# Kernel optimization log

Measured on AMD Instinct MI355X. Metric: run time of the kernel, lower is better.

## Reference

```python
import jax, jax.numpy as jnp
import numpy as np

V_K = 1.0
SIGMA = 0.1
EPS = 1e-10


def setup_inputs() -> dict:
    key = jax.random.key(0)
    ks = jax.random.split(key, 5)
    M, L, N, d, H = 2, 6, 512, 2, 64
    data = jax.random.normal(ks[0], (M, L, N, d), dtype=jnp.float32)
    t_snapshots = jnp.arange(L, dtype=jnp.float32) * 0.1
    w1 = jax.random.normal(ks[1], (H,), dtype=jnp.float32) * 0.5
    b1 = jnp.zeros((H,), jnp.float32)
    W2 = jax.random.normal(ks[2], (H, H), dtype=jnp.float32) / np.float32(np.sqrt(H))
    b2 = jnp.zeros((H,), jnp.float32)
    w3 = jax.random.normal(ks[3], (H,), dtype=jnp.float32) / np.float32(np.sqrt(H))
    b3 = jnp.zeros((), jnp.float32)
    return {"data": data, "t_snapshots": t_snapshots, "w1": w1, "b1": b1,
            "W2": W2, "b2": b2, "w3": w3, "b3": b3}


def _phi(r, w1, b1, W2, b2, w3, b3):
    # scalar-to-scalar tanh MLP applied elementwise to r (any shape)
    h1 = jnp.tanh(r[..., None] * w1 + b1)                      # [..., H]
    h2 = jnp.tanh(jnp.einsum('...h,hk->...k', h1, W2) + b2)    # [..., H]
    return jnp.einsum('...k,k->...', h2, w3) + b3              # [...]


def _loss(data, t, params):
    M, L, N, d = data.shape
    diff = data[:, :, :, None, :] - data[:, :, None, :, :]     # [M,L,N,N,d]
    ssq = jnp.sum(diff * diff, axis=-1)                        # [M,L,N,N]
    dist = jnp.where(ssq > 0, jnp.sqrt(jnp.where(ssq > 0, ssq, 1.0)), 0.0)
    off_diag = ~jnp.eye(N, dtype=bool)                         # [N,N]

    f = lambda r: _phi(r, *params)
    # Phi values on all L snapshots (for energy)
    phi = f(dist)                                              # [M,L,N,N]
    # First/second radial derivatives on current snapshots only (ell = 0..L-2)
    r_cur = dist[:, :-1]                                       # [M,L-1,N,N]
    df = lambda r: jax.jvp(f, (r,), (jnp.ones_like(r),))[1]
    dphi = df(r_cur)                                           # Phi'(r)
    d2phi = jax.jvp(df, (r_cur,), (jnp.ones_like(r_cur),))[1]  # Phi''(r)

    dt = t[1:] - t[:-1]                                        # [L-1]

    # --- drift / dissipation ---
    dist_safe = jnp.maximum(r_cur, EPS)
    unit = diff[:, :-1] / dist_safe[..., None]                 # [M,L-1,N,N,d]
    gphi = jnp.where(off_diag[..., None], dphi[..., None] * unit, 0.0)
    grad_Phi_mean = gphi.sum(axis=3) / N                       # [M,L-1,N,d]
    drift = -V_K * data[:, :-1] - grad_Phi_mean
    total_diss = ((drift ** 2).sum(axis=(2, 3)) / N * dt).sum()

    # --- laplacian / diffusion ---
    lap_phi_mean = jnp.where(off_diag, d2phi, 0.0).sum(axis=-1) / N  # [M,L-1,N]
    lap_sum = V_K * d + lap_phi_mean
    total_diff = (SIGMA ** 2 * lap_sum.mean(axis=-1) * dt).sum()

    # --- energy per snapshot ---
    V_mean = 0.5 * V_K * (data ** 2).sum(axis=-1).mean(axis=-1)      # [M,L]
    Phi_mean = jnp.where(off_diag, phi, 0.0).sum(axis=(-1, -2)) / (N * N)
    E = V_mean + Phi_mean                                            # [M,L]
    total_energy_change = (E[:, 1:] - E[:, :-1]).sum()

    n_pairs = M * (L - 1)
    residual = (total_diss + total_diff - 2.0 * total_energy_change) / n_pairs
    return residual ** 2


def reference(data, t_snapshots, w1, b1, W2, b2, w3, b3):
    return _loss(data, t_snapshots, (w1, b1, W2, b2, w3, b3))
```

## Files before the change

kernel.cpp:

```cpp
#include <hip/hip_runtime.h>
#include <hip/hip_bf16.h>

#define MM 2
#define LL 6
#define NN 512
#define HH 64
#define K_TAB 1024
#define RMAX 16.0f
#define H_STEP (RMAX / (float)K_TAB)
#define HINV   ((float)K_TAB / RMAX)


__device__ __forceinline__ float wave_reduce_sum(float v) {
    #pragma unroll
    for (int m = 32; m > 0; m >>= 1) v += __shfl_xor(v, m, 64);
    return v;
}

__global__ __launch_bounds__(256) void build_nodes(
        const float* __restrict__ w1, const float* __restrict__ b1,
        const float* __restrict__ W2, const float* __restrict__ b2,
        const float* __restrict__ w3, const float* __restrict__ b3,
        float2* __restrict__ nodes, float* __restrict__ acc) {
    int gid  = blockIdx.x * blockDim.x + threadIdx.x;
    int wave = gid >> 6;
    int lane = gid & 63;
    if (gid < 64) acc[gid] = 0.0f;
    if (wave > K_TAB) return;

    float r = (float)wave * H_STEP;

    float w1l = w1[lane];
    float u   = fmaf(r, w1l, b1[lane]);
    float t1  = tanhf(u);
    float e1  = 1.0f - t1 * t1;
    float h1  = t1;
    float h1p = e1 * w1l;

    float v = b2[lane], vp = 0.0f;
    #pragma unroll
    for (int h = 0; h < HH; ++h) {
        float a  = __shfl(h1,  h, 64);
        float ap = __shfl(h1p, h, 64);
        float w  = W2[h * HH + lane];
        v  = fmaf(a,  w, v);
        vp = fmaf(ap, w, vp);
    }
    float t2 = tanhf(v);
    float e2 = 1.0f - t2 * t2;
    float w3l = w3[lane];
    float phik = w3l * t2;
    float dpk  = w3l * e2 * vp;

    float sphi = wave_reduce_sum(phik);
    float sdp  = wave_reduce_sum(dpk);
    if (lane == 0)
        nodes[wave] = make_float2(sphi + b3[0], sdp * H_STEP);
}

__global__ __launch_bounds__(256) void pair_kernel(
        const float* __restrict__ data, const float2* __restrict__ nodes,
        float* __restrict__ acc) {
    const int blocks_per_ml = NN / 4;
    int ml = blockIdx.x / blocks_per_ml;
    int i4 = blockIdx.x % blocks_per_ml;

    __shared__ float4 coef[K_TAB];
    __shared__ float2 xs[NN];
    __shared__ float  red[4 * 4];

    #pragma unroll
    for (int e = threadIdx.x, it = 0; it < K_TAB / 256; ++it, e += 256) {
        float2 g0 = nodes[e];
        float2 g1 = nodes[e + 1];
        float  d  = g1.x - g0.x;
        coef[e] = make_float4(g0.x, g0.y,
                              3.0f * d - 2.0f * g0.y - g1.y,
                              g0.y + g1.y - 2.0f * d);
    }
    {
        const float4* src = (const float4*)(data + (size_t)ml * NN * 2);
        ((float4*)xs)[threadIdx.x] = src[threadIdx.x];
    }
    __syncthreads();

    int wv   = threadIdx.x >> 6;
    int lane = threadIdx.x & 63;
    int i    = i4 * 4 + wv;
    float2 xi = xs[i];

    float aphi = 0.0f, ad2 = 0.0f, agx = 0.0f, agy = 0.0f;
    #pragma unroll
    for (int jj = 0; jj < NN / 64; ++jj) {
        int j = jj * 64 + lane;
        float2 xj = xs[j];
        float dx = xi.x - xj.x;
        float dy = xi.y - xj.y;
        float ssq = fmaf(dx, dx, dy * dy);
        float rr  = sqrtf(ssq);
        float f   = rr * HINV;
        int   idx = (int)f;
        idx = idx > (K_TAB - 1) ? (K_TAB - 1) : idx;
        float t = f - (float)idx;
        float4 c = coef[idx];
        float phi  = fmaf(t, fmaf(t, fmaf(t, c.w, c.z), c.y), c.x);
        float dph  = fmaf(t, fmaf(t, 3.0f * c.w, 2.0f * c.z), c.y) * HINV;
        float d2ph = fmaf(t, 6.0f * c.w, 2.0f * c.z) * (HINV * HINV);
        float inv_r = 1.0f / fmaxf(rr, 1e-10f);
        bool off = (j != i);
        aphi += off ? phi  : 0.0f;
        ad2  += off ? d2ph : 0.0f;
        float s = dph * inv_r;
        agx = fmaf(s, dx, agx);
        agy = fmaf(s, dy, agy);
    }

    aphi = wave_reduce_sum(aphi);
    ad2  = wave_reduce_sum(ad2);
    agx  = wave_reduce_sum(agx);
    agy  = wave_reduce_sum(agy);

    if (lane == 0) {
        const float invN = 1.0f / (float)NN;
        float driftx = -xi.x - agx * invN;
        float drifty = -xi.y - agy * invN;
        float dr2 = fmaf(driftx, driftx, drifty * drifty);
        float vsq = fmaf(xi.x, xi.x, xi.y * xi.y);
        red[wv * 4 + 0] = aphi;
        red[wv * 4 + 1] = ad2;
        red[wv * 4 + 2] = dr2;
        red[wv * 4 + 3] = vsq;
    }
    __syncthreads();
    if (threadIdx.x < 4) {
        float s = red[0 * 4 + threadIdx.x] + red[1 * 4 + threadIdx.x]
                + red[2 * 4 + threadIdx.x] + red[3 * 4 + threadIdx.x];
        atomicAdd(&acc[ml * 4 + threadIdx.x], s);
    }
}

__global__ void finalize(const float* __restrict__ acc,
                         const float* __restrict__ t,
                         float* __restrict__ out) {
    if (threadIdx.x != 0 || blockIdx.x != 0) return;
    const double N = (double)NN;
    const double SIG2 = 0.01;
    const double VKD  = 2.0;
    double diss = 0.0, diffu = 0.0, dE = 0.0;
    for (int m = 0; m < MM; ++m) {
        double E0 = 0.0;
        for (int l = 0; l < LL; ++l) {
            int ml = m * LL + l;
            double sphi = (double)acc[ml * 4 + 0];
            double sd2  = (double)acc[ml * 4 + 1];
            double sdr  = (double)acc[ml * 4 + 2];
            double sv   = (double)acc[ml * 4 + 3];
            double E = 0.5 * sv / N + sphi / (N * N);
            if (l == 0) E0 = E;
            if (l == LL - 1) dE += E - E0;
            if (l < LL - 1) {
                double dt = (double)t[l + 1] - (double)t[l];
                diss  += sdr / N * dt;
                diffu += SIG2 * (VKD + sd2 / (N * N)) * dt;
            }
        }
    }
    double res = (diss + diffu - 2.0 * dE) / (double)(MM * (LL - 1));
    out[0] = (float)(res * res);
}

extern "C" void kernel_launch(void* const* d_in, const int* in_sizes, int n_in,
                              void* d_out, int out_size, void* d_ws, size_t ws_size,
                              hipStream_t stream) {
    const float* data = (const float*)d_in[0];
    const float* t    = (const float*)d_in[1];
    const float* w1   = (const float*)d_in[2];
    const float* b1   = (const float*)d_in[3];
    const float* W2   = (const float*)d_in[4];
    const float* b2   = (const float*)d_in[5];
    const float* w3   = (const float*)d_in[6];
    const float* b3   = (const float*)d_in[7];

    float2* nodes = (float2*)d_ws;
    float*  acc   = (float*)((char*)d_ws + 16384);

    build_nodes<<<257, 256, 0, stream>>>(w1, b1, W2, b2, w3, b3, nodes, acc);
    pair_kernel<<<MM * LL * (NN / 4), 256, 0, stream>>>(data, nodes, acc);
    finalize<<<1, 64, 0, stream>>>(acc, t, (float*)d_out);
}
```

Before: 87.38 us.

## Fuse finalize into pair kernel via last-block ticket and halve spline table

Removes the separate finalize launch by having the last pair-kernel block, found through an atomic ticket counter, compute the final scalar. The cubic Hermite table also shrinks from 1024 to 512 nodes, which halves the build_nodes work and the per-block shared-memory coefficient fill. In exchange, each block does one extra atomic and a fence, and the coarser spline lowers interpolation accuracy for phi and its derivatives.

```diff
diff --git a/kernel.cpp b/kernel.cpp
--- a/kernel.cpp
+++ b/kernel.cpp
@@ -5,7 +5,7 @@
 #define LL 6
 #define NN 512
 #define HH 64
-#define K_TAB 1024
+#define K_TAB 512
 #define RMAX 16.0f
 #define H_STEP (RMAX / (float)K_TAB)
 #define HINV   ((float)K_TAB / RMAX)
@@ -21,14 +21,16 @@
         const float* __restrict__ w1, const float* __restrict__ b1,
         const float* __restrict__ W2, const float* __restrict__ b2,
         const float* __restrict__ w3, const float* __restrict__ b3,
-        float2* __restrict__ nodes, float* __restrict__ acc) {
+        float2* __restrict__ nodes, float* __restrict__ acc,
+        int* __restrict__ ticket) {
     int gid  = blockIdx.x * blockDim.x + threadIdx.x;
-    int wave = gid >> 6;
+    int node = gid >> 6;
     int lane = gid & 63;
     if (gid < 64) acc[gid] = 0.0f;
-    if (wave > K_TAB) return;
+    if (gid == 64) *ticket = 0;
+    if (node > K_TAB) return;
 
-    float r = (float)wave * H_STEP;
+    float r = (float)node * H_STEP;
 
     float w1l = w1[lane];
     float u   = fmaf(r, w1l, b1[lane]);
@@ -49,18 +51,16 @@
     float t2 = tanhf(v);
     float e2 = 1.0f - t2 * t2;
     float w3l = w3[lane];
-    float phik = w3l * t2;
-    float dpk  = w3l * e2 * vp;
-
-    float sphi = wave_reduce_sum(phik);
-    float sdp  = wave_reduce_sum(dpk);
+    float sphi = wave_reduce_sum(w3l * t2);
+    float sdp  = wave_reduce_sum(w3l * e2 * vp);
     if (lane == 0)
-        nodes[wave] = make_float2(sphi + b3[0], sdp * H_STEP);
+        nodes[node] = make_float2(sphi + b3[0], sdp * H_STEP);
 }
 
 __global__ __launch_bounds__(256) void pair_kernel(
         const float* __restrict__ data, const float2* __restrict__ nodes,
-        float* __restrict__ acc) {
+        const float* __restrict__ t, float* __restrict__ acc,
+        int* __restrict__ ticket, float* __restrict__ out) {
     const int blocks_per_ml = NN / 4;
     int ml = blockIdx.x / blocks_per_ml;
     int i4 = blockIdx.x % blocks_per_ml;
@@ -68,9 +68,11 @@
     __shared__ float4 coef[K_TAB];
     __shared__ float2 xs[NN];
     __shared__ float  red[4 * 4];
+    __shared__ bool   is_last;
 
     #pragma unroll
-    for (int e = threadIdx.x, it = 0; it < K_TAB / 256; ++it, e += 256) {
+    for (int it = 0; it < K_TAB / 256; ++it) {
+        int e = it * 256 + threadIdx.x;
         float2 g0 = nodes[e];
         float2 g1 = nodes[e + 1];
         float  d  = g1.x - g0.x;
@@ -101,11 +103,11 @@
         float f   = rr * HINV;
         int   idx = (int)f;
         idx = idx > (K_TAB - 1) ? (K_TAB - 1) : idx;
-        float t = f - (float)idx;
+        float tt = f - (float)idx;
         float4 c = coef[idx];
-        float phi  = fmaf(t, fmaf(t, fmaf(t, c.w, c.z), c.y), c.x);
-        float dph  = fmaf(t, fmaf(t, 3.0f * c.w, 2.0f * c.z), c.y) * HINV;
-        float d2ph = fmaf(t, 6.0f * c.w, 2.0f * c.z) * (HINV * HINV);
+        float phi  = fmaf(tt, fmaf(tt, fmaf(tt, c.w, c.z), c.y), c.x);
+        float dph  = fmaf(tt, fmaf(tt, 3.0f * c.w, 2.0f * c.z), c.y) * HINV;
+        float d2ph = fmaf(tt, 6.0f * c.w, 2.0f * c.z) * (HINV * HINV);
         float inv_r = 1.0f / fmaxf(rr, 1e-10f);
         bool off = (j != i);
         aphi += off ? phi  : 0.0f;
@@ -137,36 +139,40 @@
                 + red[2 * 4 + threadIdx.x] + red[3 * 4 + threadIdx.x];
         atomicAdd(&acc[ml * 4 + threadIdx.x], s);
     }
-}
 
-__global__ void finalize(const float* __restrict__ acc,
-                         const float* __restrict__ t,
-                         float* __restrict__ out) {
-    if (threadIdx.x != 0 || blockIdx.x != 0) return;
-    const double N = (double)NN;
-    const double SIG2 = 0.01;
-    const double VKD  = 2.0;
-    double diss = 0.0, diffu = 0.0, dE = 0.0;
-    for (int m = 0; m < MM; ++m) {
-        double E0 = 0.0;
-        for (int l = 0; l < LL; ++l) {
-            int ml = m * LL + l;
-            double sphi = (double)acc[ml * 4 + 0];
-            double sd2  = (double)acc[ml * 4 + 1];
-            double sdr  = (double)acc[ml * 4 + 2];
-            double sv   = (double)acc[ml * 4 + 3];
-            double E = 0.5 * sv / N + sphi / (N * N);
-            if (l == 0) E0 = E;
-            if (l == LL - 1) dE += E - E0;
-            if (l < LL - 1) {
-                double dt = (double)t[l + 1] - (double)t[l];
-                diss  += sdr / N * dt;
-                diffu += SIG2 * (VKD + sd2 / (N * N)) * dt;
+    if (threadIdx.x == 0) {
+        __threadfence();
+        int prev = __hip_atomic_fetch_add(ticket, 1, __ATOMIC_ACQ_REL,
+                                          __HIP_MEMORY_SCOPE_AGENT);
+        is_last = (prev == (int)gridDim.x - 1);
+    }
+    __syncthreads();
+    if (is_last && threadIdx.x == 0) {
+        const double N = (double)NN;
+        const double SIG2 = 0.01;
+        const double VKD  = 2.0;
+        double diss = 0.0, diffu = 0.0, dE = 0.0;
+        for (int m = 0; m < MM; ++m) {
+            double E0 = 0.0;
+            for (int l = 0; l < LL; ++l) {
+                int idx = m * LL + l;
+                double sphi = (double)__hip_atomic_load(&acc[idx * 4 + 0], __ATOMIC_RELAXED, __HIP_MEMORY_SCOPE_AGENT);
+                double sd2  = (double)__hip_atomic_load(&acc[idx * 4 + 1], __ATOMIC_RELAXED, __HIP_MEMORY_SCOPE_AGENT);
+                double sdr  = (double)__hip_atomic_load(&acc[idx * 4 + 2], __ATOMIC_RELAXED, __HIP_MEMORY_SCOPE_AGENT);
+                double sv   = (double)__hip_atomic_load(&acc[idx * 4 + 3], __ATOMIC_RELAXED, __HIP_MEMORY_SCOPE_AGENT);
+                double E = 0.5 * sv / N + sphi / (N * N);
+                if (l == 0) E0 = E;
+                if (l == LL - 1) dE += E - E0;
+                if (l < LL - 1) {
+                    double dt = (double)t[l + 1] - (double)t[l];
+                    diss  += sdr / N * dt;
+                    diffu += SIG2 * (VKD + sd2 / (N * N)) * dt;
+                }
             }
         }
+        double res = (diss + diffu - 2.0 * dE) / (double)(MM * (LL - 1));
+        out[0] = (float)(res * res);
     }
-    double res = (diss + diffu - 2.0 * dE) / (double)(MM * (LL - 1));
-    out[0] = (float)(res * res);
 }
 
 extern "C" void kernel_launch(void* const* d_in, const int* in_sizes, int n_in,
@@ -181,10 +187,11 @@
     const float* w3   = (const float*)d_in[6];
     const float* b3   = (const float*)d_in[7];
 
-    float2* nodes = (float2*)d_ws;
-    float*  acc   = (float*)((char*)d_ws + 16384);
+    float2* nodes  = (float2*)d_ws;
+    float*  acc    = (float*)((char*)d_ws + 8192);
+    int*    ticket = (int*)((char*)d_ws + 8192 + 256);
 
-    build_nodes<<<257, 256, 0, stream>>>(w1, b1, W2, b2, w3, b3, nodes, acc);
-    pair_kernel<<<MM * LL * (NN / 4), 256, 0, stream>>>(data, nodes, acc);
-    finalize<<<1, 64, 0, stream>>>(acc, t, (float*)d_out);
+    build_nodes<<<129, 256, 0, stream>>>(w1, b1, W2, b2, w3, b3, nodes, acc, ticket);
+    pair_kernel<<<MM * LL * (NN / 4), 256, 0, stream>>>(data, nodes, t, acc, ticket,
+                                                        (float*)d_out);
 }
```

Result: slower. 116.9 us (+33.8%).
